# Kernel tuning notes

Measured on AMD Instinct MI355X. Metric: run time of the kernel, lower is better.

The kernel has to match this reference:

```python
import jax, jax.numpy as jnp
import numpy as np

NUM_NODES = 50000
NUM_EDGES = 640000
H_DIM = 128
OUT_DIM = 128
NUM_RELS = 16
NUM_BASES = 8


def _rgcn_layer(h, basis, coef, bias, src, dst, etype, norm, activation):
    # Basis decomposition: W[r] = sum_b coef[r,b] * basis[b]  -> [R, d_in, d_out]
    W = jnp.einsum('rb,bio->rio', coef, basis)
    # Transform node features under every relation: [R, N, d_out]
    Hr = jnp.einsum('ni,rio->rno', h, W)
    # Per-edge message: pick (relation, source) pair, apply edge norm. [E, d_out]
    msg = Hr[etype, src] * norm
    # Aggregate messages at destination nodes. [N, d_out]
    out = jax.ops.segment_sum(msg, dst, num_segments=h.shape[0])
    out = out + bias
    return activation(out) if activation is not None else out


def setup_inputs() -> dict:
    key = jax.random.key(0)
    ks = jax.random.split(key, 10)
    h = jax.random.normal(ks[0], (NUM_NODES, H_DIM), dtype=jnp.float32)
    norm = jax.random.uniform(ks[1], (NUM_EDGES, 1), dtype=jnp.float32)
    src = jax.random.randint(ks[2], (NUM_EDGES,), 0, NUM_NODES, dtype=jnp.int32)
    dst = jax.random.randint(ks[3], (NUM_EDGES,), 0, NUM_NODES, dtype=jnp.int32)
    etype = jax.random.randint(ks[4], (NUM_EDGES,), 0, NUM_RELS, dtype=jnp.int32)
    s1 = 1.0 / np.sqrt(H_DIM)
    s2 = 1.0 / np.sqrt(H_DIM)
    V1 = jax.random.normal(ks[5], (NUM_BASES, H_DIM, H_DIM), dtype=jnp.float32) * s1
    coef1 = jax.random.normal(ks[6], (NUM_RELS, NUM_BASES), dtype=jnp.float32) * (1.0 / np.sqrt(NUM_BASES))
    bias1 = jnp.zeros((H_DIM,), dtype=jnp.float32)
    V2 = jax.random.normal(ks[7], (NUM_BASES, H_DIM, OUT_DIM), dtype=jnp.float32) * s2
    coef2 = jax.random.normal(ks[8], (NUM_RELS, NUM_BASES), dtype=jnp.float32) * (1.0 / np.sqrt(NUM_BASES))
    bias2 = jnp.zeros((OUT_DIM,), dtype=jnp.float32)
    return {
        'h': h, 'norm': norm, 'src': src, 'dst': dst, 'etype': etype,
        'V1': V1, 'coef1': coef1, 'bias1': bias1,
        'V2': V2, 'coef2': coef2, 'bias2': bias2,
    }


def reference(h, norm, src, dst, etype, V1, coef1, bias1, V2, coef2, bias2):
    # Layer 0: relational graph conv with ReLU (hidden layer)
    h1 = _rgcn_layer(h, V1, coef1, bias1, src, dst, etype, norm, jax.nn.relu)
    # Layer 1+: BaseRGCN sorts edges by relation (bucketing for the low-mem
    # per-relation dispatch). The sort is a permutation of the edge set, so we
    # mirror it explicitly; the segment_sum result is mathematically identical.
    order = jnp.argsort(etype)
    src_s, dst_s, et_s, norm_s = src[order], dst[order], etype[order], norm[order]
    out = _rgcn_layer(h1, V2, coef2, bias2, src_s, dst_s, et_s, norm_s, None)
    return out
```

## Files before the change

### kernel.cpp

```cpp
#include <hip/hip_runtime.h>

#define N_RELS 16
#define N_BASES 8
#define HD 128
#define SCAN_B 1024
#define ROWS 16

typedef __attribute__((ext_vector_type(8))) short bf16x8;
typedef __attribute__((ext_vector_type(4))) float floatx4;
typedef __attribute__((ext_vector_type(2))) float floatx2;

__device__ __forceinline__ short bf16rn(float f) {
    union { float f; unsigned u; } v; v.f = f;
    unsigned u = v.u;
    unsigned r = (u + 0x7fffu + ((u >> 16) & 1u)) >> 16;
    return (short)r;
}

__device__ __forceinline__ unsigned packbf2(floatx2 a) {
    return ((unsigned)(unsigned short)bf16rn(a.y) << 16) | (unsigned short)bf16rn(a.x);
}


__global__ void setup_fused(const float* __restrict__ h, unsigned* __restrict__ hb, int n4,
                            const float* __restrict__ V1, const float* __restrict__ V2,
                            short* __restrict__ Vf,
                            const int* __restrict__ dst, int E, int* __restrict__ cnt,
                            int packBlocks, int vBlocks) {
    int blk = blockIdx.x;
    if (blk < packBlocks) {
        int i = blk * blockDim.x + threadIdx.x;
        if (i < n4) {
            float4 v = ((const float4*)h)[i];
            uint2 o;
            o.x = ((unsigned)(unsigned short)bf16rn(v.y) << 16) | (unsigned short)bf16rn(v.x);
            o.y = ((unsigned)(unsigned short)bf16rn(v.w) << 16) | (unsigned short)bf16rn(v.z);
            ((uint2*)hb)[i] = o;
        }
        return;
    }
    blk -= packBlocks;
    if (blk < vBlocks) {
        const float* V = ((blk & 8) ? V2 : V1) + (size_t)(blk & 7) * 16384;
        size_t obase = (size_t)blk * 16384;
        for (int e = threadIdx.x; e < 16384; e += blockDim.x) {
            float w = V[e];
            int k = e >> 7, n = e & 127;
            int kk = k >> 5, q = (k >> 3) & 3, j = k & 7;
            int lane = q * 16 + (n & 15);
            int idx = ((kk * 8 + (n >> 4)) * 64 + lane) * 8 + j;
            Vf[obase + idx] = bf16rn(w);
        }
        return;
    }
    blk -= vBlocks;
    int i = blk * blockDim.x + threadIdx.x;
    if (i < E) atomicAdd(&cnt[dst[i]], 1);
}


__global__ void scan_partial(const int* __restrict__ cnt, int N,
                             int* __restrict__ excl, int* __restrict__ bsum) {
    __shared__ int s[SCAN_B];
    int t = threadIdx.x, i = blockIdx.x * SCAN_B + t;
    int v = (i < N) ? cnt[i] : 0;
    s[t] = v; __syncthreads();
    for (int o = 1; o < SCAN_B; o <<= 1) {
        int x = (t >= o) ? s[t - o] : 0;
        __syncthreads();
        s[t] += x;
        __syncthreads();
    }
    if (i < N) excl[i] = s[t] - v;
    if (t == SCAN_B - 1) bsum[blockIdx.x] = s[t];
}

__global__ void scan_fixup(int* __restrict__ row_ptr, const int* __restrict__ bsum,
                           int nb, int N, int E, int* __restrict__ cursor) {
    __shared__ int pref[64];
    int t = threadIdx.x;
    if (t < 64) {
        int raw = (t < nb) ? bsum[t] : 0;
        int v = raw;
#pragma unroll
        for (int o = 1; o < 64; o <<= 1) {
            int u = __shfl_up(v, o, 64);
            if (t >= o) v += u;
        }
        pref[t] = v - raw;
    }
    __syncthreads();
    int i = blockIdx.x * blockDim.x + t;
    if (i < N) { int val = row_ptr[i] + pref[i >> 10]; row_ptr[i] = val; cursor[i] = val; }
    if (i == 0) row_ptr[N] = E;
}

__global__ void scatter_dst(const int* __restrict__ dst, const int* __restrict__ src,
                            const int* __restrict__ et, const float* __restrict__ norm,
                            int E, int* __restrict__ cursor, int2* __restrict__ edata) {
    int i = blockIdx.x * blockDim.x + threadIdx.x;
    if (i >= E) return;
    int p = atomicAdd(&cursor[dst[i]], 1);
    edata[p] = make_int2((et[i] << 16) | src[i], __float_as_int(norm[i]));
}


__global__ __launch_bounds__(512, 4) void rgcn_tile(
    const unsigned* __restrict__ hb, const int2* __restrict__ edata,
    const int* __restrict__ row_ptr, const float* __restrict__ coef,
    const short* __restrict__ Vf, const float* __restrict__ bias,
    void* __restrict__ outp, int N, int E, int mode) {
    __shared__ __align__(16) unsigned Zs[N_BASES][4][4][ROWS + 1][4];
    __shared__ __align__(16) float cofs[N_RELS * N_BASES];

    const int tid = threadIdx.x;
    const int wave = tid >> 6, lane = tid & 63;
    const int l32 = tid & 31;
    const int nb0 = blockIdx.x * ROWS;

    if (tid < N_RELS * N_BASES) cofs[tid] = coef[tid];
    __syncthreads();

    const int r = tid >> 5;
    const int node = nb0 + r;
    const int cn = (node < N) ? node : (N - 1);
    const int s = row_ptr[cn];
    const int len = (node < N) ? (row_ptr[cn + 1] - s) : 0;

    int mx = max(len, __shfl_xor(len, 32, 64));
    const int nG = __builtin_amdgcn_readfirstlane(mx);

    floatx2 a0[N_BASES] = {}, a1[N_BASES] = {};
    const uint2* hbp = (const uint2*)hb;

    auto edix = [&](int j) { int ix = s + j; return (ix > E - 1) ? (E - 1) : ix; };
    auto gath = [&](int2 m) { return hbp[(size_t)(m.x & 0xffff) * 32 + l32]; };
    auto proc = [&](int2 m, uint2 g, int j) {
        float nv = (j < len) ? __int_as_float(m.y) : 0.f;
        int ets = m.x >> 16;
        floatx4 c0 = *(const floatx4*)&cofs[ets * 8];
        floatx4 c1 = *(const floatx4*)&cofs[ets * 8 + 4];
        floatx2 v0, v1;
        v0.x = __uint_as_float(g.x << 16) * nv; v0.y = __uint_as_float(g.x & 0xffff0000u) * nv;
        v1.x = __uint_as_float(g.y << 16) * nv; v1.y = __uint_as_float(g.y & 0xffff0000u) * nv;
#pragma unroll
        for (int b = 0; b < N_BASES; b++) {
            float cw = (b < 4) ? c0[b] : c1[b - 4];
            a0[b] = v0 * cw + a0[b];
            a1[b] = v1 * cw + a1[b];
        }
    };

    int2 mA = edata[edix(0)], mB = edata[edix(1)], mC = edata[edix(2)];
    uint2 gA = gath(mA), gB;

    for (int k = 0; k < nG; k += 6) {
        gB = gath(mB); proc(mA, gA, k);     mA = edata[edix(k + 3)];
        gA = gath(mC); proc(mB, gB, k + 1); mB = edata[edix(k + 4)];
        gB = gath(mA); proc(mC, gA, k + 2); mC = edata[edix(k + 5)];
        gA = gath(mB); proc(mA, gB, k + 3); mA = edata[edix(k + 6)];
        gB = gath(mC); proc(mB, gA, k + 4); mB = edata[edix(k + 7)];
        gA = gath(mA); proc(mC, gB, k + 5); mC = edata[edix(k + 8)];
    }

    {
        uint2 w;
#pragma unroll
        for (int b = 0; b < N_BASES; b++) {
            w.x = packbf2(a0[b]);
            w.y = packbf2(a1[b]);
            *(uint2*)&Zs[b][l32 >> 3][(l32 >> 1) & 3][r][(l32 & 1) * 2] = w;
        }
    }
    __syncthreads();

    const int q = lane >> 4, cc = lane & 15;
    const int tt = wave;
    floatx4 ac = {};

#pragma unroll 2
    for (int b = 0; b < N_BASES; b++) {
#pragma unroll
        for (int kk = 0; kk < 4; kk++) {
            bf16x8 a = *(const bf16x8*)&Zs[b][kk][q][cc][0];
            bf16x8 B = *(const bf16x8*)(Vf + (size_t)b * 16384 +
                                        ((size_t)(kk * 8 + tt) * 64 + lane) * 8);
            ac = __builtin_amdgcn_mfma_f32_16x16x32_bf16(a, B, ac, 0, 0, 0);
        }
    }

    float bv = bias[tt * 16 + cc];
    if (mode == 0) {
        unsigned short* o = (unsigned short*)outp;
#pragma unroll
        for (int i = 0; i < 4; i++) {
            int nd = nb0 + q * 4 + i;
            if (nd < N) {
                float v = fmaxf(ac[i] + bv, 0.f);
                o[(size_t)nd * HD + tt * 16 + cc] = (unsigned short)bf16rn(v);
            }
        }
    } else {
        float* o = (float*)outp;
#pragma unroll
        for (int i = 0; i < 4; i++) {
            int nd = nb0 + q * 4 + i;
            if (nd < N) o[(size_t)nd * HD + tt * 16 + cc] = ac[i] + bv;
        }
    }
}


extern "C" void kernel_launch(void* const* d_in, const int* in_sizes, int n_in,
                              void* d_out, int out_size, void* d_ws, size_t ws_size,
                              hipStream_t stream) {
    const float* h     = (const float*)d_in[0];
    const float* norm  = (const float*)d_in[1];
    const int*   src   = (const int*)d_in[2];
    const int*   dst   = (const int*)d_in[3];
    const int*   etype = (const int*)d_in[4];
    const float* V1    = (const float*)d_in[5];
    const float* coef1 = (const float*)d_in[6];
    const float* bias1 = (const float*)d_in[7];
    const float* V2    = (const float*)d_in[8];
    const float* coef2 = (const float*)d_in[9];
    const float* bias2 = (const float*)d_in[10];
    const int N = in_sizes[0] / HD;
    const int E = in_sizes[2];
    float* out = (float*)d_out;
    (void)n_in; (void)out_size; (void)ws_size;

    char* ws = (char*)d_ws;
    size_t off = 0;
    auto alloc = [&](size_t bytes) {
        void* p = ws + off;
        off += (bytes + 255) & ~(size_t)255;
        return p;
    };
    short*    Vf      = (short*)alloc((size_t)16 * 16384 * sizeof(short));
    unsigned* hb      = (unsigned*)alloc((size_t)N * 64 * sizeof(unsigned));
    unsigned* h1b     = (unsigned*)alloc((size_t)N * 64 * sizeof(unsigned));
    int2*     edata   = (int2*)alloc((size_t)E * sizeof(int2));
    int*      cnt     = (int*)alloc((size_t)N * sizeof(int));
    int*      row_ptr = (int*)alloc((size_t)(N + 1) * sizeof(int));
    int*      cursor  = (int*)alloc((size_t)N * sizeof(int));
    int*      bsum    = (int*)alloc(256 * sizeof(int));

    const int nb = (N + SCAN_B - 1) / SCAN_B;
    const int packBlocks = (N * 32 + 255) / 256;
    const int vBlocks = 16;
    const int histBlocks = (E + 255) / 256;

    hipMemsetAsync(cnt, 0, (size_t)N * sizeof(int), stream);
    setup_fused<<<packBlocks + vBlocks + histBlocks, 256, 0, stream>>>(
        h, hb, N * 32, V1, V2, Vf, dst, E, cnt, packBlocks, vBlocks);
    scan_partial<<<nb, SCAN_B, 0, stream>>>(cnt, N, row_ptr, bsum);
    scan_fixup<<<(N + 255) / 256, 256, 0, stream>>>(row_ptr, bsum, nb, N, E, cursor);
    scatter_dst<<<(E + 255) / 256, 256, 0, stream>>>(dst, src, etype, norm, E, cursor, edata);

    const int tiles = (N + ROWS - 1) / ROWS;

    rgcn_tile<<<tiles, 512, 0, stream>>>(hb, edata, row_ptr, coef1, Vf, bias1, h1b, N, E, 0);
    rgcn_tile<<<tiles, 512, 0, stream>>>(h1b, edata, row_ptr, coef2, Vf + (size_t)8 * 16384,
                                         bias2, out, N, E, 1);
}
```

Baseline: 355.5 us.

## Sort edges by (dst, relation) and accumulate per-relation before basis mixing

The CSR build now keys edges by (destination, relation). Each destination's edges are then grouped by relation, so the gather loop keeps a single 4-float accumulator and flushes it to a per-relation LDS slot whenever the relation changes. The 8-basis coefficient mixing moves out of the per-edge loop into a 16-relation epilogue. This removes 8x FMA work per edge and lowers register pressure, in exchange for a 16x larger histogram and scan, an extra scan level, a bigger LDS tile, an LDS zero-fill, and rounding to bf16 at the per-relation partial sums. A hardware pack-to-bf16 instruction replaces the software rounding.

```diff
diff --git a/kernel.cpp b/kernel.cpp
--- a/kernel.cpp
+++ b/kernel.cpp
@@ -17,15 +17,18 @@
     return (short)r;
 }
 
-__device__ __forceinline__ unsigned packbf2(floatx2 a) {
-    return ((unsigned)(unsigned short)bf16rn(a.y) << 16) | (unsigned short)bf16rn(a.x);
+__device__ __forceinline__ unsigned cvtpk_bf16(float lo, float hi) {
+    unsigned r;
+    asm("v_cvt_pk_bf16_f32 %0, %1, %2" : "=v"(r) : "v"(lo), "v"(hi));
+    return r;
 }
 
 
 __global__ void setup_fused(const float* __restrict__ h, unsigned* __restrict__ hb, int n4,
                             const float* __restrict__ V1, const float* __restrict__ V2,
                             short* __restrict__ Vf,
-                            const int* __restrict__ dst, int E, int* __restrict__ cnt,
+                            const int* __restrict__ dst, const int* __restrict__ et,
+                            int E, int* __restrict__ cnt,
                             int packBlocks, int vBlocks) {
     int blk = blockIdx.x;
     if (blk < packBlocks) {
@@ -55,7 +58,7 @@
     }
     blk -= vBlocks;
     int i = blk * blockDim.x + threadIdx.x;
-    if (i < E) atomicAdd(&cnt[dst[i]], 1);
+    if (i < E) atomicAdd(&cnt[dst[i] * N_RELS + et[i]], 1);
 }
 
 
@@ -75,24 +78,15 @@
     if (t == SCAN_B - 1) bsum[blockIdx.x] = s[t];
 }
 
-__global__ void scan_fixup(int* __restrict__ row_ptr, const int* __restrict__ bsum,
-                           int nb, int N, int E, int* __restrict__ cursor) {
-    __shared__ int pref[64];
-    int t = threadIdx.x;
-    if (t < 64) {
-        int raw = (t < nb) ? bsum[t] : 0;
-        int v = raw;
-#pragma unroll
-        for (int o = 1; o < 64; o <<= 1) {
-            int u = __shfl_up(v, o, 64);
-            if (t >= o) v += u;
-        }
-        pref[t] = v - raw;
-    }
-    __syncthreads();
-    int i = blockIdx.x * blockDim.x + t;
-    if (i < N) { int val = row_ptr[i] + pref[i >> 10]; row_ptr[i] = val; cursor[i] = val; }
-    if (i == 0) row_ptr[N] = E;
+__global__ void fixup16(int* __restrict__ excl, const int* __restrict__ bsumE,
+                        int NK, int E, int* __restrict__ cursor) {
+    int i = blockIdx.x * blockDim.x + threadIdx.x;
+    if (i < NK) {
+        int v = excl[i] + bsumE[i >> 10];
+        excl[i] = v;
+        cursor[i] = v;
+    }
+    if (i == 0) excl[NK] = E;
 }
 
 __global__ void scatter_dst(const int* __restrict__ dst, const int* __restrict__ src,
@@ -100,76 +94,102 @@
                             int E, int* __restrict__ cursor, int2* __restrict__ edata) {
     int i = blockIdx.x * blockDim.x + threadIdx.x;
     if (i >= E) return;
-    int p = atomicAdd(&cursor[dst[i]], 1);
+    int p = atomicAdd(&cursor[dst[i] * N_RELS + et[i]], 1);
     edata[p] = make_int2((et[i] << 16) | src[i], __float_as_int(norm[i]));
 }
 
 
 __global__ __launch_bounds__(512, 4) void rgcn_tile(
     const unsigned* __restrict__ hb, const int2* __restrict__ edata,
-    const int* __restrict__ row_ptr, const float* __restrict__ coef,
+    const int* __restrict__ rp16, const float* __restrict__ coef,
     const short* __restrict__ Vf, const float* __restrict__ bias,
     void* __restrict__ outp, int N, int E, int mode) {
-    __shared__ __align__(16) unsigned Zs[N_BASES][4][4][ROWS + 1][4];
-    __shared__ __align__(16) float cofs[N_RELS * N_BASES];
+    __shared__ __align__(16) unsigned Zs[N_RELS][4][4][ROWS + 1][4];
+    __shared__ __align__(16) floatx2 cofs2[N_RELS][N_BASES];
 
     const int tid = threadIdx.x;
     const int wave = tid >> 6, lane = tid & 63;
     const int l32 = tid & 31;
     const int nb0 = blockIdx.x * ROWS;
 
-    if (tid < N_RELS * N_BASES) cofs[tid] = coef[tid];
+    for (int i = tid; i < 4352; i += 512) ((uint4*)Zs)[i] = make_uint4(0, 0, 0, 0);
+    if (tid < N_RELS * N_BASES) {
+        float c = coef[tid];
+        floatx2 p; p.x = c; p.y = c;
+        cofs2[tid >> 3][tid & 7] = p;
+    }
     __syncthreads();
 
     const int r = tid >> 5;
     const int node = nb0 + r;
     const int cn = (node < N) ? node : (N - 1);
-    const int s = row_ptr[cn];
-    const int len = (node < N) ? (row_ptr[cn + 1] - s) : 0;
+    const int s = rp16[cn * N_RELS];
+    const int len = (node < N) ? (rp16[cn * N_RELS + N_RELS] - s) : 0;
 
     int mx = max(len, __shfl_xor(len, 32, 64));
     const int nG = __builtin_amdgcn_readfirstlane(mx);
 
-    floatx2 a0[N_BASES] = {}, a1[N_BASES] = {};
+    floatx2 a0 = {}, a1 = {};
     const uint2* hbp = (const uint2*)hb;
+    unsigned* const flushp = &Zs[0][l32 >> 3][(l32 >> 1) & 3][r][(l32 & 1) * 2];
+    const int ET_STRIDE = 4 * 4 * (ROWS + 1) * 4;
 
     auto edix = [&](int j) { int ix = s + j; return (ix > E - 1) ? (E - 1) : ix; };
     auto gath = [&](int2 m) { return hbp[(size_t)(m.x & 0xffff) * 32 + l32]; };
-    auto proc = [&](int2 m, uint2 g, int j) {
-        float nv = (j < len) ? __int_as_float(m.y) : 0.f;
-        int ets = m.x >> 16;
-        floatx4 c0 = *(const floatx4*)&cofs[ets * 8];
-        floatx4 c1 = *(const floatx4*)&cofs[ets * 8 + 4];
+    auto proc = [&](int2 m, int2 mn, uint2 g, int j) {
+        const bool inr = j < len;
+        float nv = inr ? __int_as_float(m.y) : 0.f;
+        floatx2 nvp; nvp.x = nv; nvp.y = nv;
         floatx2 v0, v1;
-        v0.x = __uint_as_float(g.x << 16) * nv; v0.y = __uint_as_float(g.x & 0xffff0000u) * nv;
-        v1.x = __uint_as_float(g.y << 16) * nv; v1.y = __uint_as_float(g.y & 0xffff0000u) * nv;
+        v0.x = __uint_as_float(g.x << 16); v0.y = __uint_as_float(g.x & 0xffff0000u);
+        v1.x = __uint_as_float(g.y << 16); v1.y = __uint_as_float(g.y & 0xffff0000u);
+        a0 = v0 * nvp + a0;
+        a1 = v1 * nvp + a1;
+        int etc = m.x >> 16;
+        int etn = (j + 1 < len) ? (mn.x >> 16) : -1;
+        if (inr && etn != etc) {
+            uint2 w;
+            w.x = cvtpk_bf16(a0.x, a0.y);
+            w.y = cvtpk_bf16(a1.x, a1.y);
+            *(uint2*)(flushp + etc * ET_STRIDE) = w;
+            a0.x = 0.f; a0.y = 0.f; a1.x = 0.f; a1.y = 0.f;
+        }
+    };
+
+    int2 mA = edata[edix(0)], mB = edata[edix(1)], mC = edata[edix(2)];
+    int2 mD = edata[edix(3)], mE = edata[edix(4)], mF = edata[edix(5)];
+    uint2 gA = gath(mA), gB = gath(mB), gC;
+
+    for (int k = 0; k < nG; k += 6) {
+        gC = gath(mC); proc(mA, mB, gA, k + 0); mA = edata[edix(k + 6)];
+        gA = gath(mD); proc(mB, mC, gB, k + 1); mB = edata[edix(k + 7)];
+        gB = gath(mE); proc(mC, mD, gC, k + 2); mC = edata[edix(k + 8)];
+        gC = gath(mF); proc(mD, mE, gA, k + 3); mD = edata[edix(k + 9)];
+        gA = gath(mA); proc(mE, mF, gB, k + 4); mE = edata[edix(k + 10)];
+        gB = gath(mB); proc(mF, mA, gC, k + 5); mF = edata[edix(k + 11)];
+    }
+
+    {
+        floatx2 o0[N_BASES] = {}, o1[N_BASES] = {};
+#pragma unroll
+        for (int rr = 0; rr < N_RELS; rr++) {
+            uint2 w = *(uint2*)(flushp + rr * ET_STRIDE);
+            floatx2 v0, v1;
+            v0.x = __uint_as_float(w.x << 16); v0.y = __uint_as_float(w.x & 0xffff0000u);
+            v1.x = __uint_as_float(w.y << 16); v1.y = __uint_as_float(w.y & 0xffff0000u);
+#pragma unroll
+            for (int b = 0; b < N_BASES; b++) {
+                floatx2 cw = cofs2[rr][b];
+                o0[b] = v0 * cw + o0[b];
+                o1[b] = v1 * cw + o1[b];
+            }
+        }
 #pragma unroll
         for (int b = 0; b < N_BASES; b++) {
-            float cw = (b < 4) ? c0[b] : c1[b - 4];
-            a0[b] = v0 * cw + a0[b];
-            a1[b] = v1 * cw + a1[b];
-        }
-    };
-
-    int2 mA = edata[edix(0)], mB = edata[edix(1)], mC = edata[edix(2)];
-    uint2 gA = gath(mA), gB;
-
-    for (int k = 0; k < nG; k += 6) {
-        gB = gath(mB); proc(mA, gA, k);     mA = edata[edix(k + 3)];
-        gA = gath(mC); proc(mB, gB, k + 1); mB = edata[edix(k + 4)];
-        gB = gath(mA); proc(mC, gA, k + 2); mC = edata[edix(k + 5)];
-        gA = gath(mB); proc(mA, gB, k + 3); mA = edata[edix(k + 6)];
-        gB = gath(mC); proc(mB, gA, k + 4); mB = edata[edix(k + 7)];
-        gA = gath(mA); proc(mC, gB, k + 5); mC = edata[edix(k + 8)];
-    }
-
-    {
-        uint2 w;
-#pragma unroll
-        for (int b = 0; b < N_BASES; b++) {
-            w.x = packbf2(a0[b]);
-            w.y = packbf2(a1[b]);
-            *(uint2*)&Zs[b][l32 >> 3][(l32 >> 1) & 3][r][(l32 & 1) * 2] = w;
+            uint2 w;
+            w.x = cvtpk_bf16(o0[b].x, o0[b].y);
+            w.y = cvtpk_bf16(o1[b].x, o1[b].y);
+            *(uint2*)(flushp + b * ET_STRIDE) = w;
         }
     }
     __syncthreads();
@@ -227,6 +247,7 @@
     const float* bias2 = (const float*)d_in[10];
     const int N = in_sizes[0] / HD;
     const int E = in_sizes[2];
+    const int NK = N * N_RELS;
     float* out = (float*)d_out;
     (void)n_in; (void)out_size; (void)ws_size;
 
@@ -241,26 +262,29 @@
     unsigned* hb      = (unsigned*)alloc((size_t)N * 64 * sizeof(unsigned));
     unsigned* h1b     = (unsigned*)alloc((size_t)N * 64 * sizeof(unsigned));
     int2*     edata   = (int2*)alloc((size_t)E * sizeof(int2));
-    int*      cnt     = (int*)alloc((size_t)N * sizeof(int));
-    int*      row_ptr = (int*)alloc((size_t)(N + 1) * sizeof(int));
-    int*      cursor  = (int*)alloc((size_t)N * sizeof(int));
-    int*      bsum    = (int*)alloc(256 * sizeof(int));
-
-    const int nb = (N + SCAN_B - 1) / SCAN_B;
+    int*      cnt16   = (int*)alloc((size_t)NK * sizeof(int));
+    int*      excl16  = (int*)alloc((size_t)(NK + 1) * sizeof(int));
+    int*      cursor  = (int*)alloc((size_t)NK * sizeof(int));
+    int*      bsum    = (int*)alloc(1024 * sizeof(int));
+    int*      bsumE   = (int*)alloc(1024 * sizeof(int));
+    int*      dummy   = (int*)alloc(16 * sizeof(int));
+
+    const int nb16 = (NK + SCAN_B - 1) / SCAN_B;
     const int packBlocks = (N * 32 + 255) / 256;
     const int vBlocks = 16;
     const int histBlocks = (E + 255) / 256;
 
-    hipMemsetAsync(cnt, 0, (size_t)N * sizeof(int), stream);
+    hipMemsetAsync(cnt16, 0, (size_t)NK * sizeof(int), stream);
     setup_fused<<<packBlocks + vBlocks + histBlocks, 256, 0, stream>>>(
-        h, hb, N * 32, V1, V2, Vf, dst, E, cnt, packBlocks, vBlocks);
-    scan_partial<<<nb, SCAN_B, 0, stream>>>(cnt, N, row_ptr, bsum);
-    scan_fixup<<<(N + 255) / 256, 256, 0, stream>>>(row_ptr, bsum, nb, N, E, cursor);
+        h, hb, N * 32, V1, V2, Vf, dst, etype, E, cnt16, packBlocks, vBlocks);
+    scan_partial<<<nb16, SCAN_B, 0, stream>>>(cnt16, NK, excl16, bsum);
+    scan_partial<<<1, SCAN_B, 0, stream>>>(bsum, nb16, bsumE, dummy);
+    fixup16<<<(NK + 255) / 256, 256, 0, stream>>>(excl16, bsumE, NK, E, cursor);
     scatter_dst<<<(E + 255) / 256, 256, 0, stream>>>(dst, src, etype, norm, E, cursor, edata);
 
     const int tiles = (N + ROWS - 1) / ROWS;
 
-    rgcn_tile<<<tiles, 512, 0, stream>>>(hb, edata, row_ptr, coef1, Vf, bias1, h1b, N, E, 0);
-    rgcn_tile<<<tiles, 512, 0, stream>>>(h1b, edata, row_ptr, coef2, Vf + (size_t)8 * 16384,
+    rgcn_tile<<<tiles, 512, 0, stream>>>(hb, edata, excl16, coef1, Vf, bias1, h1b, N, E, 0);
+    rgcn_tile<<<tiles, 512, 0, stream>>>(h1b, edata, excl16, coef2, Vf + (size_t)8 * 16384,
                                          bias2, out, N, E, 1);
 }
```

Result: no change. 357.3 us (+0.5%).
